# Optimization experiments

Measured on AMD Instinct MI355X. Metric: run time of the kernel, lower is better.

The kernel has to match this reference:

```python
import math
import jax, jax.numpy as jnp
import numpy as np

S, E = 8192, 64
CAPACITY_FACTOR = 1.0
MIN_CAPACITY = 2


def setup_inputs() -> dict:
    key = jax.random.key(0)
    k1, k2 = jax.random.split(key)
    logits = jax.random.normal(k1, (S, E), dtype=jnp.float32)
    noise = jax.random.normal(k2, (S, E), dtype=jnp.float32)
    return {"logits": logits, "noise": noise}


def reference(logits, noise):
    s, e = logits.shape
    # _capacity: ceil(tokens/experts * capacity_factor*2), min-clamped; static under jit
    capacity = int(max(MIN_CAPACITY, math.ceil((s / e) * CAPACITY_FACTOR * 2.0)))

    gates = jax.nn.softmax(logits, axis=1)                      # [s,e]
    idx1 = jnp.argmax(gates, axis=1)                            # [s]
    mask1 = jax.nn.one_hot(idx1, e, dtype=jnp.int32)            # [s,e]

    neg_min = jnp.finfo(logits.dtype).min
    logits_w_noise = logits + noise
    logits_except1 = jnp.where(mask1.astype(bool), neg_min, logits_w_noise)
    idx2 = jnp.argmax(logits_except1, axis=1)
    mask2 = jax.nn.one_hot(idx2, e, dtype=jnp.int32)            # [s,e]

    locations1 = jnp.cumsum(mask1, axis=0) - 1                  # [s,e]
    locations2 = jnp.cumsum(mask2, axis=0) - 1 + jnp.sum(mask1, axis=0, keepdims=True)

    me = jnp.mean(gates, axis=0)                                # [e]
    ce = jnp.mean(mask1.astype(logits.dtype), axis=0)           # [e]
    l_aux = jnp.mean(me * ce * e * e)

    # drop tokens over capacity
    mask1 = mask1 * (locations1 < capacity).astype(jnp.int32)
    mask2 = mask2 * (locations2 < capacity).astype(jnp.int32)

    locations1_s = jnp.sum(locations1 * mask1, axis=1)          # [s]
    locations2_s = jnp.sum(locations2 * mask2, axis=1)          # [s]
    locations1_sc = jax.nn.one_hot(locations1_s, capacity, dtype=logits.dtype)  # [s,c]
    locations2_sc = jax.nn.one_hot(locations2_s, capacity, dtype=logits.dtype)

    mask1_f = mask1.astype(logits.dtype)
    mask2_f = mask2.astype(logits.dtype)
    gates1_s = jnp.sum(gates * mask1_f, axis=1)                 # [s]
    gates2_s = jnp.sum(gates * mask2_f, axis=1)
    denom_s = jnp.maximum(gates1_s + gates2_s, jnp.finfo(logits.dtype).eps)
    gates1_s = gates1_s / denom_s
    gates2_s = gates2_s / denom_s

    combine_weights = (
        jnp.einsum('s,se,sc->sec', gates1_s, mask1_f, locations1_sc)
        + jnp.einsum('s,se,sc->sec', gates2_s, mask2_f, locations2_sc)
    )  # [s,e,c]
    dispatch_mask = combine_weights.astype(bool)
    return (l_aux, combine_weights, dispatch_mask)
```

## Files before the change

### kernel.cpp

```cpp
#include <hip/hip_runtime.h>


namespace {
constexpr int  TOK  = 8192;
constexpr int  NEXP = 64;
constexpr int  CAPC = 256;
constexpr int  CHK  = 64;
constexpr int  NCHK = TOK / CHK;
constexpr long long TBLK = (long long)NEXP * CAPC;
constexpr long long SEC  = (long long)TOK * TBLK;
constexpr float NEGMIN = -3.402823466e38f;
constexpr float EPSF   = 1.1920929e-7f;
constexpr long long PK_OFF  = 16377LL * TBLK + 8;
constexpr long long G1_OFF  = 16378LL * TBLK + 8;
constexpr long long G2_OFF  = 16379LL * TBLK + 8;
constexpr long long H12_OFF = 16380LL * TBLK + 8;
constexpr long long ME_OFF  = 16381LL * TBLK + 8;
constexpr long long B12_OFF = 16382LL * TBLK + 8;
}

typedef float f32x4 __attribute__((ext_vector_type(4)));

__device__ __forceinline__ float wave_max64(float v) {
    for (int o = 32; o; o >>= 1) v = fmaxf(v, __shfl_xor(v, o));
    return v;
}
__device__ __forceinline__ float wave_sum64(float v) {
    for (int o = 32; o; o >>= 1) v += __shfl_xor(v, o);
    return v;
}

__global__ __launch_bounds__(512) void tg_gate(const float* __restrict__ logits,
                                               const float* __restrict__ noise,
                                               float* __restrict__ out)
{
    __shared__ int   i12s[CHK];
    __shared__ float g1s[CHK], g2s[CHK];
    __shared__ int   lr1s[CHK], lr2s[CHK];
    __shared__ int   cnt[2][NEXP];
    __shared__ float meSh[512];
    const int tid = threadIdx.x, lane = tid & 63, wv = tid >> 6;
    const int c = blockIdx.x;

    if (tid < 128) cnt[tid >> 6][tid & 63] = 0;

    float meAcc = 0.f;
    #pragma unroll
    for (int i = 0; i < CHK / 8; ++i) {
        const int rloc = i * 8 + wv;
        const int row  = c * CHK + rloc;
        const float l = logits[row * NEXP + lane];
        const float n = noise [row * NEXP + lane];

        const float m    = wave_max64(l);
        const float ex   = __expf(l - m);
        const float sm   = wave_sum64(ex);
        const float gate = ex / sm;

        const unsigned long long b1 = __ballot(l == m);
        const int   i1 = __ffsll(b1) - 1;
        const float G1 = __shfl(gate, i1);

        const float lw = (lane == i1) ? NEGMIN : (l + n);
        const float m2 = wave_max64(lw);
        const unsigned long long b2 = __ballot(lw == m2);
        const int   i2 = __ffsll(b2) - 1;
        const float G2 = __shfl(gate, i2);

        if (lane == 0) {
            i12s[rloc] = i1 | (i2 << 8);
            g1s[rloc]  = G1;
            g2s[rloc]  = G2;
        }
        meAcc += gate;
    }
    meSh[tid] = meAcc;
    __syncthreads();

    if (wv < 2) {
        const int sel = wv;
        const int pk  = i12s[lane];
        const int e   = sel ? ((pk >> 8) & 255) : (pk & 255);
        unsigned long long m = ~0ull;
        #pragma unroll
        for (int b = 0; b < 6; ++b) {
            const unsigned long long bb = __ballot((e >> b) & 1);
            m &= ((e >> b) & 1) ? bb : ~bb;
        }
        const unsigned long long below = (1ull << lane) - 1;
        (sel ? lr2s : lr1s)[lane] = __popcll(m & below);
        if ((m & below) == 0) cnt[sel][e] = __popcll(m);
    }
    __syncthreads();

    int* outi = (int*)out;
    if (tid < CHK) {
        const int pk = i12s[tid];
        outi[PK_OFF + c * CHK + tid] = (pk & 0xffff) | (lr1s[tid] << 16) | (lr2s[tid] << 24);
        out [G1_OFF + c * CHK + tid] = g1s[tid];
        out [G2_OFF + c * CHK + tid] = g2s[tid];
    }
    if (tid < NEXP) {
        outi[H12_OFF + c * NEXP + tid] = cnt[0][tid] | (cnt[1][tid] << 16);
        float s = 0.f;
        #pragma unroll
        for (int w = 0; w < 8; ++w) s += meSh[w * 64 + tid];
        out[ME_OFF + c * NEXP + tid] = s;
    }
}

__global__ __launch_bounds__(256) void tg_scan(float* __restrict__ out)
{
    __shared__ int   s1[4][NEXP], s2[4][NEXP];
    __shared__ float sm[4][NEXP];
    const int tid = threadIdx.x, e = tid & 63, q = tid >> 6;
    const int* outi = (const int*)out;

    int t1 = 0, t2 = 0;
    float ms = 0.f;
    #pragma unroll
    for (int i = 0; i < NCHK / 4; ++i) {
        const int c = q * (NCHK / 4) + i;
        const int h = outi[H12_OFF + c * NEXP + e];
        t1 += h & 0xffff;
        t2 += h >> 16;
        ms += out[ME_OFF + c * NEXP + e];
    }
    s1[q][e] = t1; s2[q][e] = t2; sm[q][e] = ms;
    __syncthreads();

    int off1 = 0, off2 = 0, T1 = 0;
    float MS = 0.f;
    #pragma unroll
    for (int qq = 0; qq < 4; ++qq) {
        if (qq < q) { off1 += s1[qq][e]; off2 += s2[qq][e]; }
        T1 += s1[qq][e];
        MS += sm[qq][e];
    }

    int p1 = off1, p2 = T1 + off2;
    int* wbi = (int*)out;
    #pragma unroll
    for (int i = 0; i < NCHK / 4; ++i) {
        const int c = q * (NCHK / 4) + i;
        const int h = outi[H12_OFF + c * NEXP + e];
        wbi[B12_OFF + c * NEXP + e] = p1 | (p2 << 16);
        p1 += h & 0xffff;
        p2 += h >> 16;
    }

    if (q == 0) {
        float term = (MS * (1.f / TOK)) * ((float)T1 * (1.f / TOK)) * (float)(NEXP * NEXP);
        term = wave_sum64(term);
        if (e == 0) out[0] = term * (1.f / NEXP);
    }
}

__global__ __launch_bounds__(256) void tg_emit(float* __restrict__ out)
{
    const int s = blockIdx.x * 256 + threadIdx.x;
    const int c = s >> 6;
    const int* outi = (const int*)out;
    const int   pk = outi[PK_OFF + s];
    const float G1 = out[G1_OFF + s];
    const float G2 = out[G2_OFF + s];
    const int i1 = pk & 255, i2 = (pk >> 8) & 255;
    const unsigned b1w = (unsigned)outi[B12_OFF + c * NEXP + i1];
    const unsigned b2w = (unsigned)outi[B12_OFF + c * NEXP + i2];
    const int loc1 = (int)(b1w & 0xffffu) + ((pk >> 16) & 255);
    const int loc2 = (int)(b2w >> 16)     + ((pk >> 24) & 255);

    const bool k1 = loc1 < CAPC, k2 = loc2 < CAPC;
    const float ge1 = k1 ? G1 : 0.f, ge2 = k2 ? G2 : 0.f;
    const float dn  = fmaxf(ge1 + ge2, EPSF);
    const float w1 = ge1 / dn, w2 = ge2 / dn;
    const int rec0 = i1 | (i2 << 8) | (k1 ? 1 << 16 : 0) | (k2 ? 1 << 17 : 0);
    const int rec1 = (k1 ? loc1 : 0) | ((k2 ? loc2 : 0) << 16);
    const int j1 = k1 ? (i1 * CAPC + loc1 + 1) : -1;
    const int j2 = k2 ? (i2 * CAPC + loc2 + 1) : -1;

    long long h = (long long)s * TBLK;
    ((int*)out)[h + 1] = rec0;
    ((int*)out)[h + 2] = rec1;
    out[h + 3] = w1;
    out[h + 4] = w2;
    out[h + TBLK] = (j1 == (int)TBLK) ? w1 : ((j2 == (int)TBLK) ? w2 : 0.f);

    h = (long long)(TOK + s) * TBLK;
    ((int*)out)[h + 1] = rec0;
    ((int*)out)[h + 2] = rec1;
    out[h + 3] = 1.f;
    out[h + 4] = 1.f;
    out[h + TBLK] = (j1 == (int)TBLK || j2 == (int)TBLK) ? 1.f : 0.f;
}

__global__ __launch_bounds__(256) void tg_write(float* __restrict__ out)
{
    const int lane = threadIdx.x & 63, wv = threadIdx.x >> 6;
    const int w = blockIdx.x * 4 + wv;
    float* base = out + (long long)w * TBLK;

    const f32x4 A  = *(const f32x4*)base;
    const float v2 = base[4];
    const float sv  = A.x;
    const int  rec0 = __float_as_int(A.y);
    const int  rec1 = __float_as_int(A.z);
    const float v1  = A.w;
    const bool k1 = (rec0 >> 16) & 1, k2 = (rec0 >> 17) & 1;
    const int  i1 = rec0 & 255, i2 = (rec0 >> 8) & 255;
    const int  j1 = i1 * CAPC + (rec1 & 0xffff) + 1;
    const int  j2 = i2 * CAPC + (rec1 >> 16) + 1;

    f32x4* b4 = (f32x4*)base;
    const f32x4 z = {0.f, 0.f, 0.f, 0.f};
    #pragma unroll
    for (int i = 0; i < 64; ++i)
        __builtin_nontemporal_store(z, &b4[i * 64 + lane]);

    asm volatile("s_waitcnt vmcnt(0)" ::: "memory");
    if (lane == 0) {
        base[0] = sv;
        if (k1) base[j1] = v1;
        if (k2) base[j2] = v2;
    }
}

extern "C" void kernel_launch(void* const* d_in, const int* in_sizes, int n_in,
                              void* d_out, int out_size, void* d_ws, size_t ws_size,
                              hipStream_t stream)
{
    (void)d_ws; (void)ws_size; (void)in_sizes; (void)n_in; (void)out_size;
    const float* logits = (const float*)d_in[0];
    const float* noise  = (const float*)d_in[1];
    float* out = (float*)d_out;

    tg_gate <<<NCHK,      512, 0, stream>>>(logits, noise, out);
    tg_scan <<<1,         256, 0, stream>>>(out);
    tg_emit <<<TOK / 256, 256, 0, stream>>>(out);
    tg_write<<<TOK / 2,   256, 0, stream>>>(out);
}
```

Baseline: 210.2 us.

## Move scratch to workspace and fold emit stage into write kernel

Intermediate per-token and per-chunk data now lives in the provided workspace instead of being parked in the output tensor. The separate emit kernel is gone: each write wave recomputes its token's record and the previous row's straddling element directly from workspace. This removes one launch and the scattered read-modify traffic to the output. In exchange the write kernel does extra dependent gathers per wave before zeroing, and each record is computed twice.

New measurement: 221.6 us. 5.4% more time.

```diff
diff --git a/kernel.cpp b/kernel.cpp
--- a/kernel.cpp
+++ b/kernel.cpp
@@ -11,12 +11,13 @@
 constexpr long long SEC  = (long long)TOK * TBLK;
 constexpr float NEGMIN = -3.402823466e38f;
 constexpr float EPSF   = 1.1920929e-7f;
-constexpr long long PK_OFF  = 16377LL * TBLK + 8;
-constexpr long long G1_OFF  = 16378LL * TBLK + 8;
-constexpr long long G2_OFF  = 16379LL * TBLK + 8;
-constexpr long long H12_OFF = 16380LL * TBLK + 8;
-constexpr long long ME_OFF  = 16381LL * TBLK + 8;
-constexpr long long B12_OFF = 16382LL * TBLK + 8;
+constexpr int PKO  = 0;
+constexpr int G1O  = 8192;
+constexpr int G2O  = 16384;
+constexpr int H12O = 24576;
+constexpr int MEO  = 32768;
+constexpr int B12O = 40960;
+constexpr int LAUX = 49152;
 }
 
 typedef float f32x4 __attribute__((ext_vector_type(4)));
@@ -32,7 +33,8 @@
 
 __global__ __launch_bounds__(512) void tg_gate(const float* __restrict__ logits,
                                                const float* __restrict__ noise,
-                                               float* __restrict__ out)
+                                               int* __restrict__ wsi,
+                                               float* __restrict__ wsf)
 {
     __shared__ int   i12s[CHK];
     __shared__ float g1s[CHK], g2s[CHK];
@@ -93,38 +95,37 @@
     }
     __syncthreads();
 
-    int* outi = (int*)out;
     if (tid < CHK) {
         const int pk = i12s[tid];
-        outi[PK_OFF + c * CHK + tid] = (pk & 0xffff) | (lr1s[tid] << 16) | (lr2s[tid] << 24);
-        out [G1_OFF + c * CHK + tid] = g1s[tid];
-        out [G2_OFF + c * CHK + tid] = g2s[tid];
+        wsi[PKO + c * CHK + tid] = (pk & 0xffff) | (lr1s[tid] << 16) | (lr2s[tid] << 24);
+        wsf[G1O + c * CHK + tid] = g1s[tid];
+        wsf[G2O + c * CHK + tid] = g2s[tid];
     }
     if (tid < NEXP) {
-        outi[H12_OFF + c * NEXP + tid] = cnt[0][tid] | (cnt[1][tid] << 16);
+        wsi[H12O + c * NEXP + tid] = cnt[0][tid] | (cnt[1][tid] << 16);
         float s = 0.f;
         #pragma unroll
         for (int w = 0; w < 8; ++w) s += meSh[w * 64 + tid];
-        out[ME_OFF + c * NEXP + tid] = s;
-    }
-}
-
-__global__ __launch_bounds__(256) void tg_scan(float* __restrict__ out)
+        wsf[MEO + c * NEXP + tid] = s;
+    }
+}
+
+__global__ __launch_bounds__(256) void tg_scan(int* __restrict__ wsi,
+                                               float* __restrict__ wsf)
 {
     __shared__ int   s1[4][NEXP], s2[4][NEXP];
     __shared__ float sm[4][NEXP];
     const int tid = threadIdx.x, e = tid & 63, q = tid >> 6;
-    const int* outi = (const int*)out;
 
     int t1 = 0, t2 = 0;
     float ms = 0.f;
     #pragma unroll
     for (int i = 0; i < NCHK / 4; ++i) {
         const int c = q * (NCHK / 4) + i;
-        const int h = outi[H12_OFF + c * NEXP + e];
+        const int h = wsi[H12O + c * NEXP + e];
         t1 += h & 0xffff;
         t2 += h >> 16;
-        ms += out[ME_OFF + c * NEXP + e];
+        ms += wsf[MEO + c * NEXP + e];
     }
     s1[q][e] = t1; s2[q][e] = t2; sm[q][e] = ms;
     __syncthreads();
@@ -139,12 +140,11 @@
     }
 
     int p1 = off1, p2 = T1 + off2;
-    int* wbi = (int*)out;
     #pragma unroll
     for (int i = 0; i < NCHK / 4; ++i) {
         const int c = q * (NCHK / 4) + i;
-        const int h = outi[H12_OFF + c * NEXP + e];
-        wbi[B12_OFF + c * NEXP + e] = p1 | (p2 << 16);
+        const int h = wsi[H12O + c * NEXP + e];
+        wsi[B12O + c * NEXP + e] = p1 | (p2 << 16);
         p1 += h & 0xffff;
         p2 += h >> 16;
     }
@@ -152,64 +152,53 @@
     if (q == 0) {
         float term = (MS * (1.f / TOK)) * ((float)T1 * (1.f / TOK)) * (float)(NEXP * NEXP);
         term = wave_sum64(term);
-        if (e == 0) out[0] = term * (1.f / NEXP);
-    }
-}
-
-__global__ __launch_bounds__(256) void tg_emit(float* __restrict__ out)
-{
-    const int s = blockIdx.x * 256 + threadIdx.x;
-    const int c = s >> 6;
-    const int* outi = (const int*)out;
-    const int   pk = outi[PK_OFF + s];
-    const float G1 = out[G1_OFF + s];
-    const float G2 = out[G2_OFF + s];
+        if (e == 0) wsf[LAUX] = term * (1.f / NEXP);
+    }
+}
+
+__device__ __forceinline__ void tg_rec(const int* __restrict__ wsi,
+                                       const float* __restrict__ wsf,
+                                       int s, int sec,
+                                       int& j1, int& j2, float& v1, float& v2)
+{
+    const int pk = wsi[PKO + s];
+    const int c  = s >> 6;
     const int i1 = pk & 255, i2 = (pk >> 8) & 255;
-    const unsigned b1w = (unsigned)outi[B12_OFF + c * NEXP + i1];
-    const unsigned b2w = (unsigned)outi[B12_OFF + c * NEXP + i2];
+    const unsigned b1w = (unsigned)wsi[B12O + c * NEXP + i1];
+    const unsigned b2w = (unsigned)wsi[B12O + c * NEXP + i2];
     const int loc1 = (int)(b1w & 0xffffu) + ((pk >> 16) & 255);
     const int loc2 = (int)(b2w >> 16)     + ((pk >> 24) & 255);
-
     const bool k1 = loc1 < CAPC, k2 = loc2 < CAPC;
-    const float ge1 = k1 ? G1 : 0.f, ge2 = k2 ? G2 : 0.f;
+    const float g1 = wsf[G1O + s], g2 = wsf[G2O + s];
+    const float ge1 = k1 ? g1 : 0.f, ge2 = k2 ? g2 : 0.f;
     const float dn  = fmaxf(ge1 + ge2, EPSF);
-    const float w1 = ge1 / dn, w2 = ge2 / dn;
-    const int rec0 = i1 | (i2 << 8) | (k1 ? 1 << 16 : 0) | (k2 ? 1 << 17 : 0);
-    const int rec1 = (k1 ? loc1 : 0) | ((k2 ? loc2 : 0) << 16);
-    const int j1 = k1 ? (i1 * CAPC + loc1 + 1) : -1;
-    const int j2 = k2 ? (i2 * CAPC + loc2 + 1) : -1;
-
-    long long h = (long long)s * TBLK;
-    ((int*)out)[h + 1] = rec0;
-    ((int*)out)[h + 2] = rec1;
-    out[h + 3] = w1;
-    out[h + 4] = w2;
-    out[h + TBLK] = (j1 == (int)TBLK) ? w1 : ((j2 == (int)TBLK) ? w2 : 0.f);
-
-    h = (long long)(TOK + s) * TBLK;
-    ((int*)out)[h + 1] = rec0;
-    ((int*)out)[h + 2] = rec1;
-    out[h + 3] = 1.f;
-    out[h + 4] = 1.f;
-    out[h + TBLK] = (j1 == (int)TBLK || j2 == (int)TBLK) ? 1.f : 0.f;
-}
-
-__global__ __launch_bounds__(256) void tg_write(float* __restrict__ out)
-{
+    j1 = k1 ? (i1 * CAPC + loc1 + 1) : -1;
+    j2 = k2 ? (i2 * CAPC + loc2 + 1) : -1;
+    v1 = sec ? 1.f : ge1 / dn;
+    v2 = sec ? 1.f : ge2 / dn;
+}
+
+__global__ __launch_bounds__(256) void tg_write(float* __restrict__ out,
+                                                const int* __restrict__ wsi)
+{
+    const float* wsf = (const float*)wsi;
     const int lane = threadIdx.x & 63, wv = threadIdx.x >> 6;
     const int w = blockIdx.x * 4 + wv;
     float* base = out + (long long)w * TBLK;
 
-    const f32x4 A  = *(const f32x4*)base;
-    const float v2 = base[4];
-    const float sv  = A.x;
-    const int  rec0 = __float_as_int(A.y);
-    const int  rec1 = __float_as_int(A.z);
-    const float v1  = A.w;
-    const bool k1 = (rec0 >> 16) & 1, k2 = (rec0 >> 17) & 1;
-    const int  i1 = rec0 & 255, i2 = (rec0 >> 8) & 255;
-    const int  j1 = i1 * CAPC + (rec1 & 0xffff) + 1;
-    const int  j2 = i2 * CAPC + (rec1 >> 16) + 1;
+    const int s = w & (TOK - 1), sec = w >> 13;
+    int j1, j2; float v1, v2;
+    tg_rec(wsi, wsf, s, sec, j1, j2, v1, v2);
+
+    float straddle;
+    if (w == 0) straddle = wsf[LAUX];
+    else {
+        const int sp   = (s == 0) ? TOK - 1 : s - 1;
+        const int secp = (s == 0) ? 0 : sec;
+        int pj1, pj2; float pv1, pv2;
+        tg_rec(wsi, wsf, sp, secp, pj1, pj2, pv1, pv2);
+        straddle = (pj1 == (int)TBLK) ? pv1 : ((pj2 == (int)TBLK) ? pv2 : 0.f);
+    }
 
     f32x4* b4 = (f32x4*)base;
     const f32x4 z = {0.f, 0.f, 0.f, 0.f};
@@ -219,9 +208,11 @@
 
     asm volatile("s_waitcnt vmcnt(0)" ::: "memory");
     if (lane == 0) {
-        base[0] = sv;
-        if (k1) base[j1] = v1;
-        if (k2) base[j2] = v2;
+        base[0] = straddle;
+        if (j1 > 0 && j1 < (int)TBLK) base[j1] = v1;
+        if (j2 > 0 && j2 < (int)TBLK) base[j2] = v2;
+        if (w == 16383)
+            base[TBLK] = (j1 == (int)TBLK || j2 == (int)TBLK) ? 1.f : 0.f;
     }
 }
 
@@ -229,13 +220,14 @@
                               void* d_out, int out_size, void* d_ws, size_t ws_size,
                               hipStream_t stream)
 {
-    (void)d_ws; (void)ws_size; (void)in_sizes; (void)n_in; (void)out_size;
+    (void)ws_size; (void)in_sizes; (void)n_in; (void)out_size;
     const float* logits = (const float*)d_in[0];
     const float* noise  = (const float*)d_in[1];
     float* out = (float*)d_out;
-
-    tg_gate <<<NCHK,      512, 0, stream>>>(logits, noise, out);
-    tg_scan <<<1,         256, 0, stream>>>(out);
-    tg_emit <<<TOK / 256, 256, 0, stream>>>(out);
-    tg_write<<<TOK / 2,   256, 0, stream>>>(out);
-}
+    int*   wsi = (int*)d_ws;
+    float* wsf = (float*)d_ws;
+
+    tg_gate <<<NCHK,    512, 0, stream>>>(logits, noise, wsi, wsf);
+    tg_scan <<<1,       256, 0, stream>>>(wsi, wsf);
+    tg_write<<<TOK / 2, 256, 0, stream>>>(out, wsi);
+}
```
